# Performance work log

Hardware: AMD Instinct MI355X
Metric: run time of the kernel (lower is better)

The kernel has to match this reference:

```python
import jax, jax.numpy as jnp
import numpy as np

NGRAM_SIZE = 3
MFCC_COV_FEAT_LENGTH = 91
MFCC_COV_NUM = 6
NUM_CHANNEL = 4
CHOSEN_FEAT = [547, 548, 549, 551, 554, 556, 557, 558, 559, 560, 561, 562, 563, 565,
               566, 567, 570, 576, 580, 581, 582, 583, 584, 585, 588, 593, 598, 599, 600]
POS = {f: i for i, f in enumerate(CHOSEN_FEAT)}

D = 10000   # out_dimension
L = 100     # levels
T = 2048    # time steps


def setup_inputs() -> dict:
    key = jax.random.key(0)
    ks = jax.random.split(key, 8)
    signals = jax.random.uniform(ks[0], (T, NUM_CHANNEL), dtype=jnp.float32)
    feat = jax.random.normal(ks[1], (600,), dtype=jnp.float32)
    # Random / Level embeddings are bipolar {-1,+1} hypervectors
    keys_hv = jnp.where(jax.random.uniform(ks[2], (NUM_CHANNEL, D)) < 0.5, -1.0, 1.0).astype(jnp.float32)
    level_weight = jnp.where(jax.random.uniform(ks[3], (L, D)) < 0.5, -1.0, 1.0).astype(jnp.float32)
    # 29 Sinusoid(1, D) kernels stacked: weight [29, D], bias [29, D] ~ U(0, 2pi)
    feat_w = jax.random.normal(ks[4], (len(CHOSEN_FEAT), D), dtype=jnp.float32)
    feat_b = jax.random.uniform(ks[5], (len(CHOSEN_FEAT), D), dtype=jnp.float32, maxval=2.0 * np.pi)
    # 6 Sinusoid(91, D) kernels stacked: weight [6, D, 91], bias [6, D]
    mfcc_w = jax.random.normal(ks[6], (MFCC_COV_NUM, D, MFCC_COV_FEAT_LENGTH), dtype=jnp.float32)
    mfcc_b = jax.random.uniform(ks[7], (MFCC_COV_NUM, D), dtype=jnp.float32, maxval=2.0 * np.pi)
    return dict(signals=signals, feat=feat, keys_hv=keys_hv, level_weight=level_weight,
                feat_w=feat_w, feat_b=feat_b, mfcc_w=mfcc_w, mfcc_b=mfcc_b)


def _forward(signals, feat, keys_hv, level_weight, feat_w, feat_b, mfcc_w, mfcc_b):
    Lv = level_weight.shape[0]
    # Level embedding: nearest level of value clamped to [0,1]
    idx = jnp.clip(jnp.round(jnp.clip(signals, 0.0, 1.0) * (Lv - 1)).astype(jnp.int32), 0, Lv - 1)
    embedded = level_weight[idx]                        # [T, C, D]
    # generic encoding: bind channel keys, multiset over channels
    per_t = jnp.sum(keys_hv[None, :, :] * embedded, axis=1)  # [T, D]
    # n-gram binding with permute (= roll along D)
    n = NGRAM_SIZE
    Tn = per_t.shape[0] - n + 1
    ngram = jnp.roll(per_t[0:Tn], n - 1, axis=-1)
    for i in range(1, n - 1):
        ngram = ngram * jnp.roll(per_t[i:Tn + i], n - 1 - i, axis=-1)
    ngram = ngram * per_t[n - 1:Tn + n - 1]             # [T-n+1, D]
    sample_hv = jnp.sum(ngram, axis=0)                  # multiset -> [D]

    # 29 scalar Sinusoid kernels: feat_hvs[f] uses feat[f-1]
    sel = feat[jnp.array([f - 1 for f in CHOSEN_FEAT])]          # [29]
    proj = sel[:, None] * feat_w                                  # [29, D]
    fhv = jnp.cos(proj + feat_b) * jnp.sin(proj)                  # [29, D]
    h = lambda f: fhv[POS[f]]

    # 6 MFCC Sinusoid kernels, multibind (product) over the 6 HVs
    mf = feat[:MFCC_COV_NUM * MFCC_COV_FEAT_LENGTH].reshape(MFCC_COV_NUM, MFCC_COV_FEAT_LENGTH)
    mproj = jnp.einsum('kdf,kf->kd', mfcc_w, mf)                  # [6, D]
    mhv = jnp.cos(mproj + mfcc_b) * jnp.sin(mproj)
    mfcc_hv = jnp.prod(mhv, axis=0)                               # [D]

    comb = (h(547) * h(559) * h(565)
            + h(548) * h(560) * h(566)
            + h(549) * h(561) * h(567)
            + h(551) * h(554)
            + h(556) * h(558) * h(584) * h(557) * h(585) * h(581) * h(580)
              * h(582) * h(583) * h(598) * h(600) * h(599)
            + h(562) + h(563)
            + h(570) * h(588)
            + h(576) + h(593)
            + mfcc_hv)
    sample_hv = sample_hv * comb
    # hard_quantize
    return jnp.where(sample_hv > 0, 1.0, -1.0).astype(sample_hv.dtype).ravel()


def reference(signals, feat, keys_hv, level_weight, feat_w, feat_b, mfcc_w, mfcc_b):
    return _forward(signals, feat, keys_hv, level_weight, feat_w, feat_b, mfcc_w, mfcc_b)
```

## Files before the change

kernel.cpp:

```cpp
#include <hip/hip_runtime.h>
#include <stdint.h>

#define D 10000
#define T 2048
#define TN 2046
#define NW 162
#define NCHUNK 16
#define TCHUNK 128
#define NGBLK (NW * NCHUNK)
#define MHVTH (6 * D)
#define MHVBLK ((MHVTH + 63) / 64)


__global__ __launch_bounds__(64) void kA(
    const float* __restrict__ signals,
    const float* __restrict__ feat,
    const float* __restrict__ keys,
    const float* __restrict__ lw,
    const float* __restrict__ mfcc_w,
    const float* __restrict__ mfcc_b,
    float* __restrict__ ws)
{
    const int bid = blockIdx.x;
    const int l   = threadIdx.x;

    if (bid < NGBLK) {
        __shared__ uint32_t sidx[TCHUNK + 2];
        const int w     = bid % NW;
        const int chunk = bid / NW;
        const int t0    = chunk * TCHUNK;
        const int len   = min(TCHUNK, TN - t0);
        const int rows  = len + 2;

        for (int i = l; i < rows; i += 64) {
            const float4 s = ((const float4*)signals)[t0 + i];
            uint32_t iw;
            {
                float x0 = rintf(fminf(fmaxf(s.x, 0.f), 1.f) * 99.0f);
                float x1 = rintf(fminf(fmaxf(s.y, 0.f), 1.f) * 99.0f);
                float x2 = rintf(fminf(fmaxf(s.z, 0.f), 1.f) * 99.0f);
                float x3 = rintf(fminf(fmaxf(s.w, 0.f), 1.f) * 99.0f);
                iw  = (uint32_t)(int)x0;
                iw |= (uint32_t)(int)x1 << 8;
                iw |= (uint32_t)(int)x2 << 16;
                iw |= (uint32_t)(int)x3 << 24;
            }
            sidx[i] = iw;
        }
        __syncthreads();

        const int rc = (w * 62 + l + (D - 2)) % D;
        const float k0 = keys[rc];
        const float k1 = keys[D + rc];
        const float k2 = keys[2 * D + rc];
        const float k3 = keys[3 * D + rc];

        auto row = [&](int i) -> float {
            const uint32_t iw = sidx[i];
            const int l0 = iw & 0xff;
            const int l1 = (iw >> 8) & 0xff;
            const int l2 = (iw >> 16) & 0xff;
            const int l3 = iw >> 24;
            float r = k0 * lw[l0 * D + rc];
            r = fmaf(k1, lw[l1 * D + rc], r);
            r = fmaf(k2, lw[l2 * D + rc], r);
            r = fmaf(k3, lw[l3 * D + rc], r);
            return r;
        };

        float a = row(0);
        float b = row(1);
        float accv = 0.f;
        if (len == TCHUNK) {
            #pragma unroll 4
            for (int i = 0; i < TCHUNK; ++i) {
                const float c = row(i + 2);
                const float a2 = __shfl_up(a, 2, 64);
                const float b1 = __shfl_up(b, 1, 64);
                accv = fmaf(a2 * b1, c, accv);
                a = b; b = c;
            }
        } else {
            for (int i = 0; i < len; ++i) {
                const float c = row(i + 2);
                const float a2 = __shfl_up(a, 2, 64);
                const float b1 = __shfl_up(b, 1, 64);
                accv = fmaf(a2 * b1, c, accv);
                a = b; b = c;
            }
        }
        const int outcol = w * 62 + l - 2;
        if (l >= 2 && outcol < D) ws[chunk * D + outcol] = accv;
    } else {
        const int gid = (bid - NGBLK) * 64 + l;
        if (gid < MHVTH) {
            const int k = gid / D;
            const float* __restrict__ mf   = feat + k * 91;
            const float* __restrict__ wrow = mfcc_w + (size_t)gid * 91;
            const int p = (4 - ((gid * 91) & 3)) & 3;
            float s = 0.f;
            for (int f = 0; f < p; ++f) s = fmaf(wrow[f], mf[f], s);
            const float4* __restrict__ v = (const float4*)(wrow + p);
            #pragma unroll 2
            for (int j = 0; j < 22; ++j) {
                const float4 x = v[j];
                const int f0 = p + 4 * j;
                s = fmaf(x.x, mf[f0],     s);
                s = fmaf(x.y, mf[f0 + 1], s);
                s = fmaf(x.z, mf[f0 + 2], s);
                s = fmaf(x.w, mf[f0 + 3], s);
            }
            for (int f = p + 88; f < 91; ++f) s = fmaf(wrow[f], mf[f], s);
            ws[NCHUNK * D + gid] = cosf(s + mfcc_b[gid]) * sinf(s);
        }
    }
}

__global__ __launch_bounds__(64) void kB(
    const float* __restrict__ feat,
    const float* __restrict__ feat_w,
    const float* __restrict__ feat_b,
    float* __restrict__ out,
    const float* __restrict__ ws)
{
    static const int CF[29] = {547,548,549,551,554,556,557,558,559,560,561,562,563,565,
                               566,567,570,576,580,581,582,583,584,585,588,593,598,599,600};
    const int d = blockIdx.x * 64 + threadIdx.x;
    if (d >= D) return;

    float acc = 0.f;
    #pragma unroll
    for (int c = 0; c < NCHUNK; ++c) acc += ws[c * D + d];

    const float* __restrict__ mhv = ws + NCHUNK * D;
    float mfp = mhv[d];
    #pragma unroll
    for (int k = 1; k < 6; ++k) mfp *= mhv[k * D + d];

    float h[29];
    #pragma unroll
    for (int i = 0; i < 29; ++i) {
        const float sel  = feat[CF[i] - 1];
        const float proj = sel * feat_w[i * D + d];
        h[i] = cosf(proj + feat_b[i * D + d]) * sinf(proj);
    }

    const float comb = h[0] * h[8] * h[13]
                     + h[1] * h[9] * h[14]
                     + h[2] * h[10] * h[15]
                     + h[3] * h[4]
                     + h[5] * h[7] * h[22] * h[6] * h[23] * h[19] * h[18]
                       * h[20] * h[21] * h[26] * h[28] * h[27]
                     + h[11] + h[12]
                     + h[16] * h[24]
                     + h[17] + h[25]
                     + mfp;

    const float sv = acc * comb;
    out[d] = sv > 0.f ? 1.f : -1.f;
}

extern "C" void kernel_launch(void* const* d_in, const int* in_sizes, int n_in,
                              void* d_out, int out_size, void* d_ws, size_t ws_size,
                              hipStream_t stream) {
    const float* signals = (const float*)d_in[0];
    const float* feat    = (const float*)d_in[1];
    const float* keys    = (const float*)d_in[2];
    const float* lw      = (const float*)d_in[3];
    const float* feat_w  = (const float*)d_in[4];
    const float* feat_b  = (const float*)d_in[5];
    const float* mfcc_w  = (const float*)d_in[6];
    const float* mfcc_b  = (const float*)d_in[7];
    float* ws  = (float*)d_ws;
    float* out = (float*)d_out;

    kA<<<dim3(NGBLK + MHVBLK), dim3(64), 0, stream>>>(signals, feat, keys, lw,
                                                      mfcc_w, mfcc_b, ws);
    kB<<<dim3((D + 63) / 64), dim3(64), 0, stream>>>(feat, feat_w, feat_b, out, ws);
}
```

Measured before the change: 130.1 us.

## Vectorize n-gram kernel to float4 columns per lane with 256-thread blocks

Each lane of the n-gram stage now handles four consecutive hypervector columns through float4 loads of keys and level weights, and only the neighbouring lane's elements are shuffled in for the roll. Blocks grow to 256 threads (four wavefronts, each covering 64 time steps), so the time axis is split into 32 partial chunks and kB sums 32 partials. The MFCC blocks are placed first in the grid. The aim is to cut the number of load instructions and the halo overhead per window in the gather-heavy loop, at the cost of more partial-sum traffic and fewer total blocks.

```diff
diff --git a/kernel.cpp b/kernel.cpp
--- a/kernel.cpp
+++ b/kernel.cpp
@@ -4,15 +4,17 @@
 #define D 10000
 #define T 2048
 #define TN 2046
-#define NW 162
-#define NCHUNK 16
-#define TCHUNK 128
-#define NGBLK (NW * NCHUNK)
+#define NWIN 40
+#define WSTRIDE 252
+#define TCHB 256
+#define NYB 8
+#define NCH 32
+#define NGB (NWIN * NYB)
 #define MHVTH (6 * D)
-#define MHVBLK ((MHVTH + 63) / 64)
+#define MHVBLK ((MHVTH + 255) / 256)
 
 
-__global__ __launch_bounds__(64) void kA(
+__global__ __launch_bounds__(256) void kA(
     const float* __restrict__ signals,
     const float* __restrict__ feat,
     const float* __restrict__ keys,
@@ -22,77 +24,10 @@
     float* __restrict__ ws)
 {
     const int bid = blockIdx.x;
-    const int l   = threadIdx.x;
+    const int tid = threadIdx.x;
 
-    if (bid < NGBLK) {
-        __shared__ uint32_t sidx[TCHUNK + 2];
-        const int w     = bid % NW;
-        const int chunk = bid / NW;
-        const int t0    = chunk * TCHUNK;
-        const int len   = min(TCHUNK, TN - t0);
-        const int rows  = len + 2;
-
-        for (int i = l; i < rows; i += 64) {
-            const float4 s = ((const float4*)signals)[t0 + i];
-            uint32_t iw;
-            {
-                float x0 = rintf(fminf(fmaxf(s.x, 0.f), 1.f) * 99.0f);
-                float x1 = rintf(fminf(fmaxf(s.y, 0.f), 1.f) * 99.0f);
-                float x2 = rintf(fminf(fmaxf(s.z, 0.f), 1.f) * 99.0f);
-                float x3 = rintf(fminf(fmaxf(s.w, 0.f), 1.f) * 99.0f);
-                iw  = (uint32_t)(int)x0;
-                iw |= (uint32_t)(int)x1 << 8;
-                iw |= (uint32_t)(int)x2 << 16;
-                iw |= (uint32_t)(int)x3 << 24;
-            }
-            sidx[i] = iw;
-        }
-        __syncthreads();
-
-        const int rc = (w * 62 + l + (D - 2)) % D;
-        const float k0 = keys[rc];
-        const float k1 = keys[D + rc];
-        const float k2 = keys[2 * D + rc];
-        const float k3 = keys[3 * D + rc];
-
-        auto row = [&](int i) -> float {
-            const uint32_t iw = sidx[i];
-            const int l0 = iw & 0xff;
-            const int l1 = (iw >> 8) & 0xff;
-            const int l2 = (iw >> 16) & 0xff;
-            const int l3 = iw >> 24;
-            float r = k0 * lw[l0 * D + rc];
-            r = fmaf(k1, lw[l1 * D + rc], r);
-            r = fmaf(k2, lw[l2 * D + rc], r);
-            r = fmaf(k3, lw[l3 * D + rc], r);
-            return r;
-        };
-
-        float a = row(0);
-        float b = row(1);
-        float accv = 0.f;
-        if (len == TCHUNK) {
-            #pragma unroll 4
-            for (int i = 0; i < TCHUNK; ++i) {
-                const float c = row(i + 2);
-                const float a2 = __shfl_up(a, 2, 64);
-                const float b1 = __shfl_up(b, 1, 64);
-                accv = fmaf(a2 * b1, c, accv);
-                a = b; b = c;
-            }
-        } else {
-            for (int i = 0; i < len; ++i) {
-                const float c = row(i + 2);
-                const float a2 = __shfl_up(a, 2, 64);
-                const float b1 = __shfl_up(b, 1, 64);
-                accv = fmaf(a2 * b1, c, accv);
-                a = b; b = c;
-            }
-        }
-        const int outcol = w * 62 + l - 2;
-        if (l >= 2 && outcol < D) ws[chunk * D + outcol] = accv;
-    } else {
-        const int gid = (bid - NGBLK) * 64 + l;
+    if (bid < MHVBLK) {
+        const int gid = bid * 256 + tid;
         if (gid < MHVTH) {
             const int k = gid / D;
             const float* __restrict__ mf   = feat + k * 91;
@@ -111,9 +46,84 @@
                 s = fmaf(x.w, mf[f0 + 3], s);
             }
             for (int f = p + 88; f < 91; ++f) s = fmaf(wrow[f], mf[f], s);
-            ws[NCHUNK * D + gid] = cosf(s + mfcc_b[gid]) * sinf(s);
+            ws[NCH * D + gid] = cosf(s + mfcc_b[gid]) * sinf(s);
         }
+        return;
     }
+
+    __shared__ uint32_t sidx[TCHB + 2];
+    const int nb   = bid - MHVBLK;
+    const int w    = nb % NWIN;
+    const int yb   = nb / NWIN;
+    const int t0b  = yb * TCHB;
+    const int need = min(TCHB + 2, T - t0b);
+
+    for (int i = tid; i < need; i += 256) {
+        const float4 s = ((const float4*)signals)[t0b + i];
+        uint32_t iw;
+        {
+            const float x0 = rintf(fminf(fmaxf(s.x, 0.f), 1.f) * 99.0f);
+            const float x1 = rintf(fminf(fmaxf(s.y, 0.f), 1.f) * 99.0f);
+            const float x2 = rintf(fminf(fmaxf(s.z, 0.f), 1.f) * 99.0f);
+            const float x3 = rintf(fminf(fmaxf(s.w, 0.f), 1.f) * 99.0f);
+            iw  = (uint32_t)(int)x0;
+            iw |= (uint32_t)(int)x1 << 8;
+            iw |= (uint32_t)(int)x2 << 16;
+            iw |= (uint32_t)(int)x3 << 24;
+        }
+        sidx[i] = iw;
+    }
+    __syncthreads();
+
+    const int wv    = tid >> 6;
+    const int l     = tid & 63;
+    const int chunk = yb * 4 + wv;
+    const int t0    = chunk * 64;
+    const int len   = min(64, TN - t0);
+    const int so    = wv * 64;
+
+    const int rb = (w * WSTRIDE + D - 4) % D;
+    int c0 = rb + 4 * l; if (c0 >= D) c0 -= D;
+
+    const float4 k0 = *(const float4*)(keys + 0 * D + c0);
+    const float4 k1 = *(const float4*)(keys + 1 * D + c0);
+    const float4 k2 = *(const float4*)(keys + 2 * D + c0);
+    const float4 k3 = *(const float4*)(keys + 3 * D + c0);
+
+    auto row = [&](int i) -> float4 {
+        const uint32_t iw = sidx[so + i];
+        const float4 v0 = *(const float4*)(lw + (iw & 0xffu) * D + c0);
+        const float4 v1 = *(const float4*)(lw + ((iw >> 8) & 0xffu) * D + c0);
+        const float4 v2 = *(const float4*)(lw + ((iw >> 16) & 0xffu) * D + c0);
+        const float4 v3 = *(const float4*)(lw + (iw >> 24) * D + c0);
+        float4 r;
+        r.x = fmaf(k3.x, v3.x, fmaf(k2.x, v2.x, fmaf(k1.x, v1.x, k0.x * v0.x)));
+        r.y = fmaf(k3.y, v3.y, fmaf(k2.y, v2.y, fmaf(k1.y, v1.y, k0.y * v0.y)));
+        r.z = fmaf(k3.z, v3.z, fmaf(k2.z, v2.z, fmaf(k1.z, v1.z, k0.z * v0.z)));
+        r.w = fmaf(k3.w, v3.w, fmaf(k2.w, v2.w, fmaf(k1.w, v1.w, k0.w * v0.w)));
+        return r;
+    };
+
+    float4 a = row(0);
+    float4 b = row(1);
+    float4 acc = make_float4(0.f, 0.f, 0.f, 0.f);
+
+    #pragma unroll 4
+    for (int i = 0; i < len; ++i) {
+        const float4 c = row(i + 2);
+        const float b3u = __shfl_up(b.w, 1, 64);
+        const float a2u = __shfl_up(a.z, 1, 64);
+        const float a3u = __shfl_up(a.w, 1, 64);
+        acc.x = fmaf(a2u * b3u, c.x, acc.x);
+        acc.y = fmaf(a3u * b.x, c.y, acc.y);
+        acc.z = fmaf(a.x * b.y, c.z, acc.z);
+        acc.w = fmaf(a.y * b.z, c.w, acc.w);
+        a = b; b = c;
+    }
+
+    const int ocb = w * WSTRIDE + 4 * (l - 1);
+    if (l >= 1 && ocb + 3 < D)
+        *(float4*)(ws + chunk * D + ocb) = acc;
 }
 
 __global__ __launch_bounds__(64) void kB(
@@ -130,9 +140,9 @@
 
     float acc = 0.f;
     #pragma unroll
-    for (int c = 0; c < NCHUNK; ++c) acc += ws[c * D + d];
+    for (int c = 0; c < NCH; ++c) acc += ws[c * D + d];
 
-    const float* __restrict__ mhv = ws + NCHUNK * D;
+    const float* __restrict__ mhv = ws + NCH * D;
     float mfp = mhv[d];
     #pragma unroll
     for (int k = 1; k < 6; ++k) mfp *= mhv[k * D + d];
@@ -174,7 +184,7 @@
     float* ws  = (float*)d_ws;
     float* out = (float*)d_out;
 
-    kA<<<dim3(NGBLK + MHVBLK), dim3(64), 0, stream>>>(signals, feat, keys, lw,
-                                                      mfcc_w, mfcc_b, ws);
+    kA<<<dim3(MHVBLK + NGB), dim3(256), 0, stream>>>(signals, feat, keys, lw,
+                                                     mfcc_w, mfcc_b, ws);
     kB<<<dim3((D + 63) / 64), dim3(64), 0, stream>>>(feat, feat_w, feat_b, out, ws);
 }
```

Measured after the change: 119.3 us. 1.09x faster.
